# Performance work log

Hardware: AMD Instinct MI355X
Metric: run time of the kernel (lower is better)

Reference implementation:

```python
import jax, jax.numpy as jnp
import numpy as np

N_NODES = 100000
N_EDGES = 3200000
F_IN, HIDDEN, N_CLASSES = 512, 256, 40


def setup_inputs() -> dict:
    key = jax.random.key(0)
    ks = jax.random.split(key, 8)
    x = jax.random.normal(ks[0], (N_NODES, F_IN), dtype=jnp.float32)
    edge_row = jax.random.randint(ks[1], (N_EDGES,), 0, N_NODES, dtype=jnp.int64)
    edge_col = jax.random.randint(ks[2], (N_EDGES,), 0, N_NODES, dtype=jnp.int64)
    edge_val = jax.random.uniform(ks[3], (N_EDGES,), dtype=jnp.float32)
    # Xavier-uniform-ish weights
    lim1 = float(np.sqrt(6.0 / (F_IN + HIDDEN)))
    lim2 = float(np.sqrt(6.0 / (HIDDEN + N_CLASSES)))
    W1 = jax.random.uniform(ks[4], (F_IN, HIDDEN), minval=-lim1, maxval=lim1, dtype=jnp.float32)
    b1 = jnp.zeros((HIDDEN,), dtype=jnp.float32)
    W2 = jax.random.uniform(ks[5], (HIDDEN, N_CLASSES), minval=-lim2, maxval=lim2, dtype=jnp.float32)
    b2 = jnp.zeros((N_CLASSES,), dtype=jnp.float32)
    return {"x": x, "edge_row": edge_row, "edge_col": edge_col, "edge_val": edge_val,
            "W1": W1, "b1": b1, "W2": W2, "b2": b2}


def _spmm(edge_row, edge_col, edge_val, h):
    # out[r] = sum_e val[e] * h[col[e]] for edges with row[e]==r  (a @ h)
    msg = edge_val[:, None] * h[edge_col]            # [E, F] gather + scale
    return jax.ops.segment_sum(msg, edge_row, num_segments=N_NODES)


def reference(x, edge_row, edge_col, edge_val, W1, b1, W2, b2):
    # Layer 1: dense mm -> spmm -> bias -> relu (dropout in eval mode = identity)
    h = _spmm(edge_row, edge_col, edge_val, x @ W1) + b1
    h = jax.nn.relu(h)
    # Layer 2: dense mm -> spmm -> bias
    logits = _spmm(edge_row, edge_col, edge_val, h @ W2) + b2
    return jax.nn.log_softmax(logits, axis=1)
```

## Files before the change

kernel.cpp:

```cpp
#include <hip/hip_runtime.h>
#include <math.h>

#define NN  100000
#define NE  3200000
#define FIN 512
#define HID 256
#define NC  40

#define NBUK 391
#define SPB  9472
#define BIN_BLOCKS 782
#define CHUNK 4096
#define COLMASK 0x1FFFF

typedef __attribute__((ext_vector_type(8))) short short8;
typedef __attribute__((ext_vector_type(4))) float f32x4;

__device__ inline float bf2f(unsigned short u) {
    unsigned int x = ((unsigned int)u) << 16;
    return __builtin_bit_cast(float, x);
}
__device__ inline unsigned short f2bfu(float f) {
    unsigned int x = __builtin_bit_cast(unsigned int, f);
    unsigned int r = (x + 0x7fffu + ((x >> 16) & 1u)) >> 16;
    return (unsigned short)r;
}
__device__ inline signed char q8(float v, float s) {
    int q = (int)rintf(v * s);
    q = max(-127, min(127, q));
    return (signed char)q;
}
__device__ inline unsigned cvtpk_bf16(float lo, float hi) {
    unsigned r;
    asm("v_cvt_pk_bf16_f32 %0, %1, %2" : "=v"(r) : "v"(lo), "v"(hi));
    return r;
}
__device__ inline float cub0(int r) { float f; asm("v_cvt_f32_ubyte0 %0, %1" : "=v"(f) : "v"(r)); return f; }
__device__ inline float cub1(int r) { float f; asm("v_cvt_f32_ubyte1 %0, %1" : "=v"(f) : "v"(r)); return f; }
__device__ inline float cub2(int r) { float f; asm("v_cvt_f32_ubyte2 %0, %1" : "=v"(f) : "v"(r)); return f; }
__device__ inline float cub3(int r) { float f; asm("v_cvt_f32_ubyte3 %0, %1" : "=v"(f) : "v"(r)); return f; }

__global__ __launch_bounds__(256) void k_bin(const int* __restrict__ er, const int* __restrict__ ec,
                                             const float* __restrict__ ev, int* __restrict__ bcnt,
                                             int2* __restrict__ spack) {
    __shared__ int hist[392];
    __shared__ int lscan[392];
    __shared__ int gbase[NBUK];
    __shared__ int lcur[NBUK];
    __shared__ int sm[256];
    __shared__ int2 ebuf[CHUNK];
    __shared__ unsigned short bbuf[CHUNK];
    const int tid = threadIdx.x;
    for (int i = tid; i < 392; i += 256) hist[i] = 0;
    for (int i = tid; i < NBUK; i += 256) lcur[i] = 0;
    __syncthreads();
    const int start = blockIdx.x * CHUNK;
    const int end = min(start + CHUNK, NE);
    const int n = end - start;
    for (int e = start + tid; e < end; e += 256)
        atomicAdd(&hist[er[e] >> 8], 1);
    __syncthreads();
    int a = (2 * tid < 392) ? hist[2 * tid] : 0;
    int b = (2 * tid + 1 < 392) ? hist[2 * tid + 1] : 0;
    int v = a + b;
    sm[tid] = v;
    __syncthreads();
    for (int off = 1; off < 256; off <<= 1) {
        int t2 = (tid >= off) ? sm[tid - off] : 0;
        __syncthreads();
        sm[tid] += t2;
        __syncthreads();
    }
    int ex = sm[tid] - v;
    if (2 * tid < 392) lscan[2 * tid] = ex;
    if (2 * tid + 1 < 392) lscan[2 * tid + 1] = ex + a;
    for (int i = tid; i < NBUK; i += 256) {
        int h = hist[i];
        gbase[i] = h ? atomicAdd(&bcnt[i], h) : 0;
    }
    __syncthreads();
    for (int e = start + tid; e < end; e += 256) {
        int r = er[e];
        int bk = r >> 8;
        int lpos = atomicAdd(&lcur[bk], 1);
        int pos = lscan[bk] + lpos;
        int2 p;
        p.x = ((r & 255) << 17) | ec[e];
        p.y = __builtin_bit_cast(int, ev[e]);
        ebuf[pos] = p;
        bbuf[pos] = (unsigned short)bk;
    }
    __syncthreads();
    for (int i = tid; i < n; i += 256) {
        int bk = bbuf[i];
        spack[(size_t)bk * SPB + gbase[bk] + (i - lscan[bk])] = ebuf[i];
    }
}

__global__ __launch_bounds__(256) void k_finecsr(const int2* __restrict__ spack, const int* __restrict__ bcnt,
                                                 int2* __restrict__ cpack,
                                                 int* __restrict__ row_beg, int* __restrict__ row_cnt) {
    __shared__ int cnt[256];
    __shared__ int sm[256];
    __shared__ int cur[256];
    int tid = threadIdx.x;
    int buk = blockIdx.x;
    size_t bb = (size_t)buk * SPB;
    int n = min(bcnt[buk], SPB);
    cnt[tid] = 0;
    __syncthreads();
    for (int i = tid; i < n; i += 256) {
        int lr = ((unsigned)spack[bb + i].x) >> 17;
        atomicAdd(&cnt[lr], 1);
    }
    __syncthreads();
    int v = cnt[tid];
    sm[tid] = v;
    __syncthreads();
    for (int off = 1; off < 256; off <<= 1) {
        int t = (tid >= off) ? sm[tid - off] : 0;
        __syncthreads();
        sm[tid] += t;
        __syncthreads();
    }
    int ex = sm[tid] - v;
    cur[tid] = ex;
    int grow = buk * 256 + tid;
    if (grow < NN) {
        row_beg[grow] = (int)bb + ex;
        row_cnt[grow] = v;
    }
    __syncthreads();
    for (int i = tid; i < n; i += 256) {
        int2 p = spack[bb + i];
        int lr = ((unsigned)p.x) >> 17;
        int pos = atomicAdd(&cur[lr], 1);
        int2 q;
        q.x = p.x & COLMASK;
        q.y = p.y;
        cpack[bb + pos] = q;
    }
}

__global__ __launch_bounds__(256) void k_w1t(const float* __restrict__ W1, unsigned short* __restrict__ W1T) {
    int b = blockIdx.x;
    int n = threadIdx.x;
    unsigned short tmp[16];
#pragma unroll
    for (int kk = 0; kk < 16; kk++)
        tmp[kk] = f2bfu(W1[(size_t)(b * 16 + kk) * HID + n]);
    unsigned short* dst = W1T + (size_t)n * FIN + b * 16;
    *(short8*)dst = *(short8*)tmp;
    *(short8*)(dst + 8) = *(short8*)(tmp + 8);
}

__global__ __launch_bounds__(256) void k_w2t(const float* __restrict__ W2, unsigned short* __restrict__ W2T) {
    int n = blockIdx.x;
    int k = threadIdx.x;
    float v = (n < NC) ? W2[(size_t)k * NC + n] : 0.f;
    W2T[(size_t)n * HID + k] = f2bfu(v);
}

__global__ __launch_bounds__(512) void k_gemm1(const float* __restrict__ x, const unsigned short* __restrict__ W1T,
                                               unsigned char* __restrict__ h1) {
    __shared__ unsigned short As[2][128][40];
    __shared__ unsigned short Bs[2][256][40];
    const int tid = threadIdx.x;
    const int row0 = blockIdx.x * 128;
    const int lane = tid & 63;
    const int w = tid >> 6;
    const int wr = (w >> 2) * 64;
    const int wc = (w & 3) * 64;
    const int m16 = lane & 15;
    const int quad = lane >> 4;

    const int arow = tid >> 2;
    const int akoff = (tid & 3) * 8;
    int gar = row0 + arow;
    if (gar >= NN) gar = NN - 1;
    const float* ax = x + (size_t)gar * FIN + akoff;
    const int brow = tid >> 1;
    const int bkoff = (tid & 1) * 16;
    const unsigned short* bw = W1T + (size_t)brow * FIN + bkoff;

    f32x4 acc[4][4];
#pragma unroll
    for (int i = 0; i < 4; i++)
#pragma unroll
        for (int j = 0; j < 4; j++) acc[i][j] = (f32x4){0.f, 0.f, 0.f, 0.f};

    float4 va0, va1;
    uint4 vb0, vb1;

#define G1_LOAD(tt)                                                        \
    {                                                                      \
        const float* ap = ax + (tt) * 32;                                  \
        va0 = *(const float4*)(ap);                                        \
        va1 = *(const float4*)(ap + 4);                                    \
        const unsigned short* bp = bw + (tt) * 32;                         \
        vb0 = *(const uint4*)(bp);                                         \
        vb1 = *(const uint4*)(bp + 8);                                     \
    }

#define G1_STORE(bf)                                                       \
    {                                                                      \
        uint4 pa;                                                          \
        pa.x = cvtpk_bf16(va0.x, va0.y);                                   \
        pa.y = cvtpk_bf16(va0.z, va0.w);                                   \
        pa.z = cvtpk_bf16(va1.x, va1.y);                                   \
        pa.w = cvtpk_bf16(va1.z, va1.w);                                   \
        *(uint4*)(&As[bf][arow][akoff]) = pa;                              \
        *(uint4*)(&Bs[bf][brow][bkoff]) = vb0;                             \
        *(uint4*)(&Bs[bf][brow][bkoff + 8]) = vb1;                         \
    }

    G1_LOAD(0)
    G1_STORE(0)
    G1_LOAD(1)
    __syncthreads();

    for (int t = 0; t < 16; ++t) {
        const int buf = t & 1;
        short8 af[4], bfr[4];
#pragma unroll
        for (int i = 0; i < 4; i++) af[i] = *(const short8*)(&As[buf][wr + i * 16 + m16][quad * 8]);
#pragma unroll
        for (int j = 0; j < 4; j++) bfr[j] = *(const short8*)(&Bs[buf][wc + j * 16 + m16][quad * 8]);
        if (t < 15) {
            G1_STORE(buf ^ 1)
            if (t < 14) G1_LOAD(t + 2)
        }
#pragma unroll
        for (int i = 0; i < 4; i++)
#pragma unroll
            for (int j = 0; j < 4; j++)
                acc[i][j] = __builtin_amdgcn_mfma_f32_16x16x32_bf16(af[i], bfr[j], acc[i][j], 0, 0, 0);
        __syncthreads();
    }
#undef G1_LOAD
#undef G1_STORE

#pragma unroll
    for (int i = 0; i < 4; i++) {
#pragma unroll
        for (int r = 0; r < 4; r++) {
            int gr = row0 + wr + i * 16 + quad * 4 + r;
            if (gr < NN) {
#pragma unroll
                for (int j = 0; j < 4; j++) {
                    int c = wc + j * 16 + m16;
                    h1[(size_t)gr * HID + c] = (unsigned char)(q8(acc[i][j][r], 16.f) + 128);
                }
            }
        }
    }
}

__global__ __launch_bounds__(256) void k_spmm1(const unsigned char* __restrict__ h1,
                                               const int2* __restrict__ cpack,
                                               const int* __restrict__ row_beg, const int* __restrict__ row_cnt,
                                               const float* __restrict__ b1, unsigned short* __restrict__ a1) {
    const int lane = threadIdx.x & 63;
    const int row = (int)__builtin_amdgcn_readfirstlane(blockIdx.x * 4 + (threadIdx.x >> 6));
    if (row >= NN) return;
    const int beg = (int)__builtin_amdgcn_readfirstlane(row_beg[row]);
    const int cnt = (int)__builtin_amdgcn_readfirstlane(row_cnt[row]);
    const int end = beg + cnt;
    const int voff = lane * 4;
    float su[4] = {0.f, 0.f, 0.f, 0.f};
    float sv = 0.f;

    for (int e0 = beg; e0 < end; e0 += 16) {
        unsigned cb[16];
        float vv[16];
#pragma unroll
        for (int j = 0; j < 16; j++) {
            int idx = e0 + j;
            int cl = idx < end ? idx : end - 1;
            int2 p = cpack[cl];
            cb[j] = ((unsigned)p.x & COLMASK) << 8;
            vv[j] = idx < end ? __builtin_bit_cast(float, p.y) * 0.0625f : 0.f;
        }
        int g[16];
#pragma unroll
        for (int j = 0; j < 16; j++)
            g[j] = *(const int*)(h1 + (size_t)cb[j] + voff);
#pragma unroll
        for (int j = 0; j < 16; j++) {
            sv += vv[j];
            su[0] = fmaf(vv[j], cub0(g[j]), su[0]);
            su[1] = fmaf(vv[j], cub1(g[j]), su[1]);
            su[2] = fmaf(vv[j], cub2(g[j]), su[2]);
            su[3] = fmaf(vv[j], cub3(g[j]), su[3]);
        }
    }

    const int col = lane * 4;
    const float4 bb = *(const float4*)(b1 + col);
    ushort4 o;
    o.x = f2bfu(fmaxf(fmaf(-128.f, sv, su[0]) + bb.x, 0.f));
    o.y = f2bfu(fmaxf(fmaf(-128.f, sv, su[1]) + bb.y, 0.f));
    o.z = f2bfu(fmaxf(fmaf(-128.f, sv, su[2]) + bb.z, 0.f));
    o.w = f2bfu(fmaxf(fmaf(-128.f, sv, su[3]) + bb.w, 0.f));
    *(ushort4*)(a1 + (size_t)row * HID + col) = o;
}

__global__ __launch_bounds__(256) void k_gemm2(const unsigned short* __restrict__ a1,
                                               const unsigned short* __restrict__ W2T, unsigned char* __restrict__ h2) {
    const int tid = threadIdx.x;
    const int lane = tid & 63;
    const int w = tid >> 6;
    const int m16 = lane & 15;
    const int quad = lane >> 4;
    const int r0 = blockIdx.x * 256 + w * 64;

    f32x4 acc[4][3];
#pragma unroll
    for (int i = 0; i < 4; i++)
#pragma unroll
        for (int j = 0; j < 3; j++) acc[i][j] = (f32x4){0.f, 0.f, 0.f, 0.f};

    for (int k0 = 0; k0 < HID; k0 += 32) {
        short8 af[4], bfr[3];
#pragma unroll
        for (int i = 0; i < 4; i++) {
            int gr = r0 + i * 16 + m16;
            if (gr >= NN) gr = NN - 1;
            af[i] = *(const short8*)(a1 + (size_t)gr * HID + k0 + quad * 8);
        }
#pragma unroll
        for (int j = 0; j < 3; j++)
            bfr[j] = *(const short8*)(W2T + (size_t)(j * 16 + m16) * HID + k0 + quad * 8);
#pragma unroll
        for (int i = 0; i < 4; i++)
#pragma unroll
            for (int j = 0; j < 3; j++)
                acc[i][j] = __builtin_amdgcn_mfma_f32_16x16x32_bf16(af[i], bfr[j], acc[i][j], 0, 0, 0);
    }
#pragma unroll
    for (int i = 0; i < 4; i++) {
#pragma unroll
        for (int r = 0; r < 4; r++) {
            int gr = r0 + i * 16 + quad * 4 + r;
            if (gr < NN) {
#pragma unroll
                for (int j = 0; j < 3; j++) {
                    int c = j * 16 + m16;
                    if (c < NC) h2[(size_t)gr * 64 + c] = (unsigned char)(q8(acc[i][j][r], 4.f) + 128);
                }
            }
        }
    }
}

__global__ __launch_bounds__(256) void k_spmm2(const unsigned char* __restrict__ h2,
                                               const int2* __restrict__ cpack,
                                               const int* __restrict__ row_beg, const int* __restrict__ row_cnt,
                                               const float* __restrict__ b2, float* __restrict__ out) {
    const int lane = threadIdx.x & 63;
    const int slot = lane >> 4;
    const int t = lane & 15;
    const int row = (int)__builtin_amdgcn_readfirstlane(blockIdx.x * 4 + (threadIdx.x >> 6));
    if (row >= NN) return;
    const int beg = (int)__builtin_amdgcn_readfirstlane(row_beg[row]);
    const int cnt = (int)__builtin_amdgcn_readfirstlane(row_cnt[row]);
    const int end = beg + cnt;
    const int t4 = t * 4;
    float su[4] = {0.f, 0.f, 0.f, 0.f};
    float sv = 0.f;

    for (int e0 = beg; e0 < end; e0 += 32) {
        unsigned cb[8];
        float vs[8];
#pragma unroll
        for (int u = 0; u < 8; u++) {
            int idx = e0 + u * 4 + slot;
            int cl = idx < end ? idx : end - 1;
            int2 p = cpack[cl];
            cb[u] = ((unsigned)p.x & COLMASK) << 6;
            vs[u] = idx < end ? __builtin_bit_cast(float, p.y) * 0.25f : 0.f;
        }
        int g[8];
#pragma unroll
        for (int u = 0; u < 8; u++)
            g[u] = *(const int*)(h2 + (size_t)cb[u] + t4);
#pragma unroll
        for (int u = 0; u < 8; u++) {
            sv += vs[u];
            su[0] = fmaf(vs[u], cub0(g[u]), su[0]);
            su[1] = fmaf(vs[u], cub1(g[u]), su[1]);
            su[2] = fmaf(vs[u], cub2(g[u]), su[2]);
            su[3] = fmaf(vs[u], cub3(g[u]), su[3]);
        }
    }

#pragma unroll
    for (int i = 0; i < 4; i++) {
        su[i] += __shfl_xor(su[i], 16, 64);
        su[i] += __shfl_xor(su[i], 32, 64);
    }
    sv += __shfl_xor(sv, 16, 64);
    sv += __shfl_xor(sv, 32, 64);

    const bool act = t < 10;
    const int off = t4;
    const int boff = act ? off : 0;
    const float4 bb = *(const float4*)(b2 + boff);
    float acc[4];
    acc[0] = fmaf(-128.f, sv, su[0]) + bb.x;
    acc[1] = fmaf(-128.f, sv, su[1]) + bb.y;
    acc[2] = fmaf(-128.f, sv, su[2]) + bb.z;
    acc[3] = fmaf(-128.f, sv, su[3]) + bb.w;
    float mx = act ? fmaxf(fmaxf(acc[0], acc[1]), fmaxf(acc[2], acc[3])) : -INFINITY;
#pragma unroll
    for (int o = 1; o < 16; o <<= 1) mx = fmaxf(mx, __shfl_xor(mx, o, 16));
    float se = 0.f;
    if (act) {
#pragma unroll
        for (int i = 0; i < 4; i++) se += expf(acc[i] - mx);
    }
#pragma unroll
    for (int o = 1; o < 16; o <<= 1) se += __shfl_xor(se, o, 16);
    const float ls = logf(se);
    if (act && slot == 0) {
        float4 r;
        r.x = acc[0] - mx - ls;
        r.y = acc[1] - mx - ls;
        r.z = acc[2] - mx - ls;
        r.w = acc[3] - mx - ls;
        *(float4*)(out + (size_t)row * NC + off) = r;
    }
}

extern "C" void kernel_launch(void* const* d_in, const int* in_sizes, int n_in, void* d_out, int out_size,
                              void* d_ws, size_t ws_size, hipStream_t stream) {
    const float* x  = (const float*)d_in[0];
    const int*   er = (const int*)d_in[1];
    const int*   ec = (const int*)d_in[2];
    const float* ev = (const float*)d_in[3];
    const float* W1 = (const float*)d_in[4];
    const float* b1 = (const float*)d_in[5];
    const float* W2 = (const float*)d_in[6];
    const float* b2 = (const float*)d_in[7];
    float* out = (float*)d_out;
    char* ws = (char*)d_ws;

    int2*  spack       = (int2*)(ws + 0);
    unsigned char* h1  = (unsigned char*)(ws + 0);
    unsigned short* a1 = (unsigned short*)(ws + 29628416);
    unsigned char* h2  = (unsigned char*)(ws + 80828416);
    int2*  cpack       = (int2*)(ws + 87228416);
    int*   row_beg     = (int*)(ws + 116856832);
    int*   row_cnt     = (int*)(ws + 117256832);
    int*   bcnt        = (int*)(ws + 117656832);
    unsigned short* W1T = (unsigned short*)(ws + 117658880);
    unsigned short* W2T = (unsigned short*)(ws + 117921024);

    hipMemsetAsync(bcnt, 0, NBUK * sizeof(int), stream);
    k_w1t<<<32, 256, 0, stream>>>(W1, W1T);
    k_w2t<<<48, 256, 0, stream>>>(W2, W2T);
    k_bin<<<BIN_BLOCKS, 256, 0, stream>>>(er, ec, ev, bcnt, spack);
    k_finecsr<<<NBUK, 256, 0, stream>>>(spack, bcnt, cpack, row_beg, row_cnt);
    k_gemm1<<<782, 512, 0, stream>>>(x, W1T, h1);
    k_spmm1<<<NN / 4, 256, 0, stream>>>(h1, cpack, row_beg, row_cnt, b1, a1);
    k_gemm2<<<(NN + 255) / 256, 256, 0, stream>>>(a1, W2T, h2);
    k_spmm2<<<NN / 4, 256, 0, stream>>>(h2, cpack, row_beg, row_cnt, b2, out);
}
```

Baseline: 631.9 us.

## Merge prep kernels, retile gemm1 to 64x128 single-buffer, trim spmm edge clamping

Folds the W1/W2 transposes and the bucket-counter memset into one prep kernel, removing two launches and a memset. gemm1 is retiled from 128x256 with 512 threads and double-buffered LDS to 64x128 with 256 threads, single-buffered, and four blocks per CU, trading LDS double buffering for more resident blocks. The spmm kernels stop clamping edge indices when loading cpack, batch the loads, and move the value scaling into the epilogue. The unclamped loads can read past the end of a row's edges, or past the end of cpack for the last rows; those values are masked to zero but the reads still happen.

```diff
diff --git a/kernel.cpp b/kernel.cpp
--- a/kernel.cpp
+++ b/kernel.cpp
@@ -39,6 +39,28 @@
 __device__ inline float cub1(int r) { float f; asm("v_cvt_f32_ubyte1 %0, %1" : "=v"(f) : "v"(r)); return f; }
 __device__ inline float cub2(int r) { float f; asm("v_cvt_f32_ubyte2 %0, %1" : "=v"(f) : "v"(r)); return f; }
 __device__ inline float cub3(int r) { float f; asm("v_cvt_f32_ubyte3 %0, %1" : "=v"(f) : "v"(r)); return f; }
+
+__global__ __launch_bounds__(256) void k_prep(const float* __restrict__ W1, unsigned short* __restrict__ W1T,
+                                              const float* __restrict__ W2, unsigned short* __restrict__ W2T,
+                                              int* __restrict__ bcnt) {
+    const int b = blockIdx.x;
+    const int tid = threadIdx.x;
+    if (b < 32) {
+        unsigned short tmp[16];
+#pragma unroll
+        for (int kk = 0; kk < 16; kk++)
+            tmp[kk] = f2bfu(W1[(size_t)(b * 16 + kk) * HID + tid]);
+        unsigned short* dst = W1T + (size_t)tid * FIN + b * 16;
+        *(short8*)dst = *(short8*)tmp;
+        *(short8*)(dst + 8) = *(short8*)(tmp + 8);
+    } else if (b < 80) {
+        int n = b - 32;
+        float v = (n < NC) ? W2[(size_t)tid * NC + n] : 0.f;
+        W2T[(size_t)n * HID + tid] = f2bfu(v);
+    } else {
+        for (int i = tid; i < NBUK; i += 256) bcnt[i] = 0;
+    }
+}
 
 __global__ __launch_bounds__(256) void k_bin(const int* __restrict__ er, const int* __restrict__ ec,
                                              const float* __restrict__ ev, int* __restrict__ bcnt,
@@ -142,35 +164,17 @@
     }
 }
 
-__global__ __launch_bounds__(256) void k_w1t(const float* __restrict__ W1, unsigned short* __restrict__ W1T) {
-    int b = blockIdx.x;
-    int n = threadIdx.x;
-    unsigned short tmp[16];
-#pragma unroll
-    for (int kk = 0; kk < 16; kk++)
-        tmp[kk] = f2bfu(W1[(size_t)(b * 16 + kk) * HID + n]);
-    unsigned short* dst = W1T + (size_t)n * FIN + b * 16;
-    *(short8*)dst = *(short8*)tmp;
-    *(short8*)(dst + 8) = *(short8*)(tmp + 8);
-}
-
-__global__ __launch_bounds__(256) void k_w2t(const float* __restrict__ W2, unsigned short* __restrict__ W2T) {
-    int n = blockIdx.x;
-    int k = threadIdx.x;
-    float v = (n < NC) ? W2[(size_t)k * NC + n] : 0.f;
-    W2T[(size_t)n * HID + k] = f2bfu(v);
-}
-
-__global__ __launch_bounds__(512) void k_gemm1(const float* __restrict__ x, const unsigned short* __restrict__ W1T,
-                                               unsigned char* __restrict__ h1) {
-    __shared__ unsigned short As[2][128][40];
-    __shared__ unsigned short Bs[2][256][40];
+__global__ __launch_bounds__(256, 4) void k_gemm1(const float* __restrict__ x, const unsigned short* __restrict__ W1T,
+                                                  unsigned char* __restrict__ h1) {
+    __shared__ unsigned short As[64][40];
+    __shared__ unsigned short Bs[128][40];
     const int tid = threadIdx.x;
-    const int row0 = blockIdx.x * 128;
+    const int row0 = (blockIdx.x >> 1) * 64;
+    const int col0 = (blockIdx.x & 1) * 128;
     const int lane = tid & 63;
     const int w = tid >> 6;
-    const int wr = (w >> 2) * 64;
-    const int wc = (w & 3) * 64;
+    const int wr = (w >> 1) * 32;
+    const int wc = (w & 1) * 64;
     const int m16 = lane & 15;
     const int quad = lane >> 4;
 
@@ -181,11 +185,11 @@
     const float* ax = x + (size_t)gar * FIN + akoff;
     const int brow = tid >> 1;
     const int bkoff = (tid & 1) * 16;
-    const unsigned short* bw = W1T + (size_t)brow * FIN + bkoff;
-
-    f32x4 acc[4][4];
-#pragma unroll
-    for (int i = 0; i < 4; i++)
+    const unsigned short* bw = W1T + (size_t)(col0 + brow) * FIN + bkoff;
+
+    f32x4 acc[2][4];
+#pragma unroll
+    for (int i = 0; i < 2; i++)
 #pragma unroll
         for (int j = 0; j < 4; j++) acc[i][j] = (f32x4){0.f, 0.f, 0.f, 0.f};
 
@@ -202,53 +206,52 @@
         vb1 = *(const uint4*)(bp + 8);                                     \
     }
 
-#define G1_STORE(bf)                                                       \
+#define G1_STORE()                                                         \
     {                                                                      \
         uint4 pa;                                                          \
         pa.x = cvtpk_bf16(va0.x, va0.y);                                   \
         pa.y = cvtpk_bf16(va0.z, va0.w);                                   \
         pa.z = cvtpk_bf16(va1.x, va1.y);                                   \
         pa.w = cvtpk_bf16(va1.z, va1.w);                                   \
-        *(uint4*)(&As[bf][arow][akoff]) = pa;                              \
-        *(uint4*)(&Bs[bf][brow][bkoff]) = vb0;                             \
-        *(uint4*)(&Bs[bf][brow][bkoff + 8]) = vb1;                         \
+        *(uint4*)(&As[arow][akoff]) = pa;                                  \
+        *(uint4*)(&Bs[brow][bkoff]) = vb0;                                 \
+        *(uint4*)(&Bs[brow][bkoff + 8]) = vb1;                             \
     }
 
     G1_LOAD(0)
-    G1_STORE(0)
-    G1_LOAD(1)
+    G1_STORE()
     __syncthreads();
 
     for (int t = 0; t < 16; ++t) {
-        const int buf = t & 1;
-        short8 af[4], bfr[4];
-#pragma unroll
-        for (int i = 0; i < 4; i++) af[i] = *(const short8*)(&As[buf][wr + i * 16 + m16][quad * 8]);
-#pragma unroll
-        for (int j = 0; j < 4; j++) bfr[j] = *(const short8*)(&Bs[buf][wc + j * 16 + m16][quad * 8]);
-        if (t < 15) {
-            G1_STORE(buf ^ 1)
-            if (t < 14) G1_LOAD(t + 2)
-        }
-#pragma unroll
-        for (int i = 0; i < 4; i++)
+        if (t < 15) G1_LOAD(t + 1)
+        short8 af[2], bfr[4];
+#pragma unroll
+        for (int i = 0; i < 2; i++) af[i] = *(const short8*)(&As[wr + i * 16 + m16][quad * 8]);
+#pragma unroll
+        for (int j = 0; j < 4; j++) bfr[j] = *(const short8*)(&Bs[wc + j * 16 + m16][quad * 8]);
+#pragma unroll
+        for (int i = 0; i < 2; i++)
 #pragma unroll
             for (int j = 0; j < 4; j++)
                 acc[i][j] = __builtin_amdgcn_mfma_f32_16x16x32_bf16(af[i], bfr[j], acc[i][j], 0, 0, 0);
-        __syncthreads();
+        if (t < 15) {
+            __syncthreads();
+            G1_STORE()
+            __syncthreads();
+        }
     }
 #undef G1_LOAD
 #undef G1_STORE
 
 #pragma unroll
-    for (int i = 0; i < 4; i++) {
+    for (int i = 0; i < 2; i++) {
 #pragma unroll
         for (int r = 0; r < 4; r++) {
             int gr = row0 + wr + i * 16 + quad * 4 + r;
             if (gr < NN) {
 #pragma unroll
                 for (int j = 0; j < 4; j++) {
-                    int c = wc + j * 16 + m16;
+                    int c = col0 + wc + j * 16 + m16;
                     h1[(size_t)gr * HID + c] = (unsigned char)(q8(acc[i][j][r], 16.f) + 128);
                 }
             }
@@ -271,15 +274,16 @@
     float sv = 0.f;
 
     for (int e0 = beg; e0 < end; e0 += 16) {
+        int2 p[16];
+#pragma unroll
+        for (int j = 0; j < 16; j++)
+            p[j] = cpack[e0 + j];
         unsigned cb[16];
         float vv[16];
 #pragma unroll
         for (int j = 0; j < 16; j++) {
-            int idx = e0 + j;
-            int cl = idx < end ? idx : end - 1;
-            int2 p = cpack[cl];
-            cb[j] = ((unsigned)p.x & COLMASK) << 8;
-            vv[j] = idx < end ? __builtin_bit_cast(float, p.y) * 0.0625f : 0.f;
+            cb[j] = ((unsigned)p[j].x & COLMASK) << 8;
+            vv[j] = (e0 + j) < end ? __builtin_bit_cast(float, p[j].y) : 0.f;
         }
         int g[16];
 #pragma unroll
@@ -298,10 +302,10 @@
     const int col = lane * 4;
     const float4 bb = *(const float4*)(b1 + col);
     ushort4 o;
-    o.x = f2bfu(fmaxf(fmaf(-128.f, sv, su[0]) + bb.x, 0.f));
-    o.y = f2bfu(fmaxf(fmaf(-128.f, sv, su[1]) + bb.y, 0.f));
-    o.z = f2bfu(fmaxf(fmaf(-128.f, sv, su[2]) + bb.z, 0.f));
-    o.w = f2bfu(fmaxf(fmaf(-128.f, sv, su[3]) + bb.w, 0.f));
+    o.x = f2bfu(fmaxf(fmaf(0.0625f, fmaf(-128.f, sv, su[0]), bb.x), 0.f));
+    o.y = f2bfu(fmaxf(fmaf(0.0625f, fmaf(-128.f, sv, su[1]), bb.y), 0.f));
+    o.z = f2bfu(fmaxf(fmaf(0.0625f, fmaf(-128.f, sv, su[2]), bb.z), 0.f));
+    o.w = f2bfu(fmaxf(fmaf(0.0625f, fmaf(-128.f, sv, su[3]), bb.w), 0.f));
     *(ushort4*)(a1 + (size_t)row * HID + col) = o;
 }
 
@@ -375,10 +379,9 @@
 #pragma unroll
         for (int u = 0; u < 8; u++) {
             int idx = e0 + u * 4 + slot;
-            int cl = idx < end ? idx : end - 1;
-            int2 p = cpack[cl];
+            int2 p = cpack[idx];
             cb[u] = ((unsigned)p.x & COLMASK) << 6;
-            vs[u] = idx < end ? __builtin_bit_cast(float, p.y) * 0.25f : 0.f;
+            vs[u] = idx < end ? __builtin_bit_cast(float, p.y) : 0.f;
         }
         int g[8];
 #pragma unroll
@@ -407,10 +410,10 @@
     const int boff = act ? off : 0;
     const float4 bb = *(const float4*)(b2 + boff);
     float acc[4];
-    acc[0] = fmaf(-128.f, sv, su[0]) + bb.x;
-    acc[1] = fmaf(-128.f, sv, su[1]) + bb.y;
-    acc[2] = fmaf(-128.f, sv, su[2]) + bb.z;
-    acc[3] = fmaf(-128.f, sv, su[3]) + bb.w;
+    acc[0] = fmaf(0.25f, fmaf(-128.f, sv, su[0]), bb.x);
+    acc[1] = fmaf(0.25f, fmaf(-128.f, sv, su[1]), bb.y);
+    acc[2] = fmaf(0.25f, fmaf(-128.f, sv, su[2]), bb.z);
+    acc[3] = fmaf(0.25f, fmaf(-128.f, sv, su[3]), bb.w);
     float mx = act ? fmaxf(fmaxf(acc[0], acc[1]), fmaxf(acc[2], acc[3])) : -INFINITY;
 #pragma unroll
     for (int o = 1; o < 16; o <<= 1) mx = fmaxf(mx, __shfl_xor(mx, o, 16));
@@ -456,12 +459,10 @@
     unsigned short* W1T = (unsigned short*)(ws + 117658880);
     unsigned short* W2T = (unsigned short*)(ws + 117921024);
 
-    hipMemsetAsync(bcnt, 0, NBUK * sizeof(int), stream);
-    k_w1t<<<32, 256, 0, stream>>>(W1, W1T);
-    k_w2t<<<48, 256, 0, stream>>>(W2, W2T);
+    k_prep<<<81, 256, 0, stream>>>(W1, W1T, W2, W2T, bcnt);
     k_bin<<<BIN_BLOCKS, 256, 0, stream>>>(er, ec, ev, bcnt, spack);
     k_finecsr<<<NBUK, 256, 0, stream>>>(spack, bcnt, cpack, row_beg, row_cnt);
-    k_gemm1<<<782, 512, 0, stream>>>(x, W1T, h1);
+    k_gemm1<<<3126, 256, 0, stream>>>(x, W1T, h1);
     k_spmm1<<<NN / 4, 256, 0, stream>>>(h1, cpack, row_beg, row_cnt, b1, a1);
     k_gemm2<<<(NN + 255) / 256, 256, 0, stream>>>(a1, W2T, h2);
     k_spmm2<<<NN / 4, 256, 0, stream>>>(h2, cpack, row_beg, row_cnt, b2, out);
```

Result: slower. 673.1 us (+6.5%).
